# Kernel tuning notes

Measured on AMD Instinct MI355X. Metric: run time of the kernel, lower is better.

Reference implementation:

```python
import jax, jax.numpy as jnp
import numpy as np

B, C, T, W, H = 32, 80, 2048, 128, 512
FRAMES_PER_WORD = T // W  # 16
K = 5  # conv kernel size (Component approximated as Conv1d(k=5)+ReLU)


def conv1d(x, w, b):
    # x: [B, Cin, T], w: [Cout, Cin, K] -> [B, Cout, T] (SAME padding)
    y = jax.lax.conv_general_dilated(
        x, w, window_strides=(1,), padding='SAME',
        dimension_numbers=('NCH', 'OIH', 'NCH'))
    return y + b[None, :, None]


def setup_inputs() -> dict:
    key = jax.random.key(0)
    k1, k2, k3 = jax.random.split(key, 3)
    features = jax.random.normal(k1, (B, C, T), dtype=jnp.float32)
    # word bounds: contiguous equal-length spans [start, end) covering all T frames
    starts = (jnp.arange(W, dtype=jnp.int64) * FRAMES_PER_WORD)
    ends = starts + FRAMES_PER_WORD
    word_bounds = jnp.broadcast_to(jnp.stack([starts, ends])[None], (B, 2, W))
    word_lengths = jnp.full((B,), W, dtype=jnp.int64)
    enc_w = jax.random.normal(k2, (H, C, K), dtype=jnp.float32) * 0.02
    enc_b = jnp.zeros((H,), dtype=jnp.float32)
    dec_w = jax.random.normal(k3, (1, H, K), dtype=jnp.float32) * 0.02
    dec_b = jnp.zeros((1,), dtype=jnp.float32)
    return {'features': features, 'word_bounds': word_bounds,
            'word_lengths': word_lengths, 'enc_w': enc_w, 'enc_b': enc_b,
            'dec_w': dec_w, 'dec_b': dec_b}


def reference(features, word_bounds, word_lengths, enc_w, enc_b, dec_w, dec_b):
    # Frame encoder: Conv1d + ReLU -> [B, H, T]
    frame_embedding = jax.nn.relu(conv1d(features, enc_w, enc_b))
    t = jnp.arange(T)
    start = word_bounds[:, 0, :]  # [B, W]
    end = word_bounds[:, 1, :]    # [B, W]
    # Ragged per-word mean pooling, fused as a masked matmul (segment mean).
    mask = (t[None, None, :] >= start[..., None]) & (t[None, None, :] < end[..., None])  # [B, W, T]
    valid = jnp.arange(W)[None, :] < word_lengths[:, None]  # [B, W]
    maskf = (mask & valid[..., None]).astype(frame_embedding.dtype)
    counts = jnp.maximum(maskf.sum(-1), 1.0)  # [B, W]
    word_embeddings = jnp.einsum('bct,bwt->bcw', frame_embedding, maskf) / counts[:, None, :]
    # Word decoder: Conv1d over the word axis -> [B, 1, W]
    return conv1d(word_embeddings, dec_w, dec_b)
```

## Files before the change

### kernel.cpp

```cpp
#include <hip/hip_runtime.h>

#define B_ 32
#define C_ 80
#define T_ 2048
#define W_ 128
#define H_ 512
#define K_ 5

#define KTOT 400
#define KPAD 416
#define NKI  13
#define TM   128
#define TN   128
#define SF_STRIDE 88
#define SF_ROWS   136
#define ITER_STRIDE (2 * 4 * 64 * 8)
#define BF_ELEMS  (4 * NKI * ITER_STRIDE)

#define RB_FEAT   1024
#define RB_BFRAG  (RB_FEAT + BF_ELEMS / 256)
#define RB_WORDS  (RB_BFRAG + B_)
#define RB_WZERO  (RB_WORDS + 128)

typedef _Float16 half8 __attribute__((ext_vector_type(8)));
typedef float    f4v   __attribute__((ext_vector_type(4)));

__global__ __launch_bounds__(256) void prep_all(
    const float* __restrict__ feat, const float* __restrict__ enc_w,
    const int* __restrict__ bounds, const int* __restrict__ lengths,
    _Float16* __restrict__ featT, _Float16* __restrict__ Bf,
    int* __restrict__ word_of, float* __restrict__ inv_cnt,
    float* __restrict__ wemb)
{
    __shared__ _Float16 tile[64 * 80];
    const int bid = blockIdx.x;
    const int tid = threadIdx.x;

    if (bid < RB_FEAT) {
        const int b = bid >> 5, tc = bid & 31;
        const int t0 = tc * 64;
        for (int idx = tid; idx < 80 * 64; idx += 256) {
            int cc = idx >> 6, tt = idx & 63;
            float v = feat[((size_t)b * C_ + cc) * T_ + t0 + tt];
            tile[tt * 80 + cc] = (_Float16)v;
        }
        __syncthreads();
        for (int idx = tid; idx < 64 * 10; idx += 256) {
            int tt = idx / 10, g = idx % 10;
            *(f4v*)(featT + ((size_t)b * T_ + t0 + tt) * C_ + g * 8) =
                *(const f4v*)(tile + tt * 80 + g * 8);
        }
    } else if (bid < RB_BFRAG) {
        int idx = (bid - RB_FEAT) * 256 + tid;
        int e  = idx & 7;
        int l  = (idx >> 3) & 63;
        int j  = (idx >> 9) & 3;
        int w2 = (idx >> 11) & 1;
        int it = (idx >> 12) % NKI;
        int nt = idx / (NKI << 12);
        int h  = nt * 128 + w2 * 64 + j * 16 + (l & 15);
        int kc = it * 32 + (l >> 4) * 8 + e;
        float v = 0.f;
        if (kc < KTOT) v = enc_w[(h * C_ + kc % 80) * K_ + kc / 80];
        Bf[idx] = (_Float16)v;
    } else if (bid < RB_WORDS) {
        const int b = bid - RB_BFRAG;
        int* wob = word_of + b * T_;
        for (int t = tid; t < T_; t += 256) wob[t] = -1;
        __syncthreads();
        if (tid < W_) {
            const int len = lengths[b];
            int s = bounds[(b * 2 + 0) * W_ + tid];
            int e = bounds[(b * 2 + 1) * W_ + tid];
            s = max(s, 0); e = min(e, T_);
            bool valid = (tid < len) && (e > s);
            inv_cnt[b * W_ + tid] = valid ? 1.f / (float)(e - s) : 0.f;
            if (valid)
                for (int t = s; t < e; ++t) wob[t] = tid;
        }
    } else {
        f4v* wz = (f4v*)wemb;
        int base = (bid - RB_WORDS) * 256 + tid;
        for (int i = base; i < (B_ * W_ * H_) / 4; i += 128 * 256) wz[i] = (f4v){};
    }
}

__global__ __launch_bounds__(256, 3) void gemm_enc(
    const _Float16* __restrict__ featT,
    const _Float16* __restrict__ Bf,
    const float*    __restrict__ enc_b,
    const int*      __restrict__ word_of,
    const float*    __restrict__ inv_cnt,
    float*          __restrict__ wemb)
{
    __shared__ _Float16 sf[SF_ROWS * SF_STRIDE];

    const int tid = threadIdx.x;
    const int bid = blockIdx.x;
    const int nt = bid & 3;
    const int mt = (bid >> 2) & 15;
    const int b  = bid >> 6;
    const int t0 = mt * TM;
    const int h0 = nt * TN;

    const _Float16* fb = featT + (size_t)b * T_ * C_;
    for (int idx = tid; idx < SF_ROWS * 10; idx += 256) {
        int tt = idx / 10, g = idx % 10;
        int t = t0 - 2 + tt;
        int tcl = min(max(t, 0), T_ - 1);
        f4v v = {};
        if (t >= 0 && t < T_) v = *(const f4v*)(fb + tcl * C_ + g * 8);
        *(f4v*)(sf + tt * SF_STRIDE + g * 8) = v;
    }

    const int lane = tid & 63;
    const int wid  = tid >> 6;
    const int wm = (wid >> 1) * 64;
    const int wn = (wid & 1) * 64;
    const int w2 = wid & 1;
    const int ml = lane & 15;
    const int q  = lane >> 4;

    const half8* bfp = (const half8*)(Bf + (((nt * NKI) * 2 + w2) * 4 * 64 + lane) * 8);

    f4v acc[4][4] = {};

    __syncthreads();

    int c = q * 8;
    int aoff = (wm + ml) * SF_STRIDE + c;

    half8 bcur[4];
    #pragma unroll
    for (int j = 0; j < 4; ++j) bcur[j] = bfp[j * 64];

    for (int it = 0; it < NKI; ++it) {
        half8 bnext[4];
        {
            const half8* bn = bfp + (it + 1) * (2 * 4 * 64);
            #pragma unroll
            for (int j = 0; j < 4; ++j) bnext[j] = bn[j * 64];
        }
        half8 af[4];
        #pragma unroll
        for (int i = 0; i < 4; ++i)
            af[i] = *(const half8*)(sf + aoff + i * 16 * SF_STRIDE);
        #pragma unroll
        for (int i = 0; i < 4; ++i)
            #pragma unroll
            for (int j = 0; j < 4; ++j)
                acc[i][j] = __builtin_amdgcn_mfma_f32_16x16x32_f16(af[i], bcur[j], acc[i][j], 0, 0, 0);
        #pragma unroll
        for (int j = 0; j < 4; ++j) bcur[j] = bnext[j];
        aoff += 32; c += 32;
        if (c >= 80) { c -= 80; aoff += 8; }
    }

    const int bT = b * T_;
    const int bW = b * W_;
    float bias[4];
    #pragma unroll
    for (int j = 0; j < 4; ++j) bias[j] = enc_b[h0 + wn + j * 16 + ml];

    #pragma unroll
    for (int i = 0; i < 4; ++i) {
        const int tg = t0 + wm + i * 16;
        const int w0  = word_of[bT + tg];
        const int w15 = word_of[bT + tg + 15];
        if (w0 == w15) {
            if (w0 >= 0) {
                const float inv = inv_cnt[bW + w0];
                const bool own_lo = (tg == 0) || (word_of[bT + tg - 1] != w0);
                const bool own_hi = (tg + 16 >= T_) || (word_of[bT + tg + 16] != w0);
                #pragma unroll
                for (int j = 0; j < 4; ++j) {
                    float s = 0.f;
                    #pragma unroll
                    for (int r = 0; r < 4; ++r) s += fmaxf(acc[i][j][r] + bias[j], 0.f);
                    s += __shfl_down(s, 32, 64);
                    s += __shfl_down(s, 16, 64);
                    if (q == 0) {
                        float val = s * inv;
                        float* dst = &wemb[(size_t)(bW + w0) * H_ + h0 + wn + j * 16 + ml];
                        if (own_lo && own_hi) *dst = val;
                        else atomicAdd(dst, val);
                    }
                }
            }
        } else {
            #pragma unroll
            for (int j = 0; j < 4; ++j) {
                #pragma unroll
                for (int r = 0; r < 4; ++r) {
                    int t = tg + q * 4 + r;
                    int w = word_of[bT + t];
                    if (w >= 0)
                        atomicAdd(&wemb[(size_t)(bW + w) * H_ + h0 + wn + j * 16 + ml],
                                  fmaxf(acc[i][j][r] + bias[j], 0.f) * inv_cnt[bW + w]);
                }
            }
        }
    }
}

__global__ __launch_bounds__(256) void dec_all(const float* __restrict__ wemb,
                                               const float* __restrict__ dec_w,
                                               const float* __restrict__ dec_b,
                                               float* __restrict__ out) {
    __shared__ float sdw[H_ * K_];
    __shared__ float se[36][8];
    const int bid = blockIdx.x;
    const int b = bid >> 2, ch = bid & 3;
    const int w0 = ch * 32;
    for (int idx = threadIdx.x; idx < H_ * K_; idx += 256) sdw[idx] = dec_w[idx];
    __syncthreads();
    const int wid = threadIdx.x >> 6, lane = threadIdx.x & 63;
    for (int row = wid; row < 36; row += 4) {
        int wq = w0 - 2 + row;
        float a[K_] = {};
        if (wq >= 0 && wq < W_) {
            const float* src = wemb + ((size_t)b * W_ + wq) * H_;
            #pragma unroll
            for (int r = 0; r < H_ / 64; ++r) {
                int h = r * 64 + lane;
                float v = src[h];
                #pragma unroll
                for (int k = 0; k < K_; ++k) a[k] += v * sdw[h * K_ + k];
            }
        }
        #pragma unroll
        for (int k = 0; k < K_; ++k) {
            #pragma unroll
            for (int off = 32; off > 0; off >>= 1) a[k] += __shfl_down(a[k], off, 64);
        }
        if (lane == 0) {
            #pragma unroll
            for (int k = 0; k < K_; ++k) se[row][k] = a[k];
        }
    }
    __syncthreads();
    if (threadIdx.x < 32) {
        int wl = threadIdx.x;
        float acc = dec_b[0];
        #pragma unroll
        for (int k = 0; k < K_; ++k) acc += se[wl + k][k];
        out[b * W_ + w0 + wl] = acc;
    }
}

extern "C" void kernel_launch(void* const* d_in, const int* in_sizes, int n_in,
                              void* d_out, int out_size, void* d_ws, size_t ws_size,
                              hipStream_t stream) {
    const float* feat    = (const float*)d_in[0];
    const int*   bounds  = (const int*)  d_in[1];
    const int*   lengths = (const int*)  d_in[2];
    const float* enc_w   = (const float*)d_in[3];
    const float* enc_b   = (const float*)d_in[4];
    const float* dec_w   = (const float*)d_in[5];
    const float* dec_b   = (const float*)d_in[6];
    float* out = (float*)d_out;

    char* p = (char*)d_ws;
    _Float16* featT = (_Float16*)p;  p += (size_t)B_ * T_ * C_ * 2;
    _Float16* Bf    = (_Float16*)p;  p += (size_t)(BF_ELEMS + ITER_STRIDE) * 2;
    int* word_of    = (int*)p;       p += (size_t)B_ * T_ * 4;
    float* inv_cnt  = (float*)p;     p += (size_t)B_ * W_ * 4;
    float* wemb     = (float*)p;

    prep_all<<<RB_WZERO, 256, 0, stream>>>(feat, enc_w, bounds, lengths,
                                           featT, Bf, word_of, inv_cnt, wemb);
    gemm_enc<<<B_ * (T_ / TM) * (H_ / TN), 256, 0, stream>>>(
        featT, Bf, enc_b, word_of, inv_cnt, wemb);
    dec_all<<<B_ * 4, 256, 0, stream>>>(wemb, dec_w, dec_b, out);
}
```

Measured before the change: 130.0 us.

## Loop all N tiles per block and switch to 32x32x16 MFMA

The encoder GEMM now runs one block per (batch, 128-frame tile) and loops over all four 128-wide H tiles inside the block. The feature tile is staged in shared memory once and reused across every output column instead of being reloaded by four separate blocks. The MFMA shape moves from 16x16x32 to 32x32x16, and the weight fragment layout in prep is regenerated to match. The grid shrinks by 4x, which cuts redundant LDS staging but reduces parallelism and drops the B-fragment prefetch double buffering.

```diff
diff --git a/kernel.cpp b/kernel.cpp
--- a/kernel.cpp
+++ b/kernel.cpp
@@ -8,14 +8,12 @@
 #define K_ 5
 
 #define KTOT 400
-#define KPAD 416
 #define NKI  13
 #define TM   128
 #define TN   128
 #define SF_STRIDE 88
 #define SF_ROWS   136
-#define ITER_STRIDE (2 * 4 * 64 * 8)
-#define BF_ELEMS  (4 * NKI * ITER_STRIDE)
+#define BF_ELEMS  (4 * NKI * 2 * 2 * 2 * 64 * 8)
 
 #define RB_FEAT   1024
 #define RB_BFRAG  (RB_FEAT + BF_ELEMS / 256)
@@ -24,6 +22,7 @@
 
 typedef _Float16 half8 __attribute__((ext_vector_type(8)));
 typedef float    f4v   __attribute__((ext_vector_type(4)));
+typedef float    f16v  __attribute__((ext_vector_type(16)));
 
 __global__ __launch_bounds__(256) void prep_all(
     const float* __restrict__ feat, const float* __restrict__ enc_w,
@@ -54,14 +53,15 @@
         int idx = (bid - RB_FEAT) * 256 + tid;
         int e  = idx & 7;
         int l  = (idx >> 3) & 63;
-        int j  = (idx >> 9) & 3;
-        int w2 = (idx >> 11) & 1;
+        int j  = (idx >> 9) & 1;
+        int w2 = (idx >> 10) & 1;
+        int h  = (idx >> 11) & 1;
         int it = (idx >> 12) % NKI;
         int nt = idx / (NKI << 12);
-        int h  = nt * 128 + w2 * 64 + j * 16 + (l & 15);
-        int kc = it * 32 + (l >> 4) * 8 + e;
+        int n  = nt * 128 + w2 * 64 + j * 32 + (l & 31);
+        int kc = it * 32 + h * 16 + (l >> 5) * 8 + e;
         float v = 0.f;
-        if (kc < KTOT) v = enc_w[(h * C_ + kc % 80) * K_ + kc / 80];
+        if (kc < KTOT) v = enc_w[(n * C_ + kc % 80) * K_ + kc / 80];
         Bf[idx] = (_Float16)v;
     } else if (bid < RB_WORDS) {
         const int b = bid - RB_BFRAG;
@@ -97,11 +97,9 @@
 
     const int tid = threadIdx.x;
     const int bid = blockIdx.x;
-    const int nt = bid & 3;
-    const int mt = (bid >> 2) & 15;
-    const int b  = bid >> 6;
+    const int mt = bid & 15;
+    const int b  = bid >> 4;
     const int t0 = mt * TM;
-    const int h0 = nt * TN;
 
     const _Float16* fb = featT + (size_t)b * T_ * C_;
     for (int idx = tid; idx < SF_ROWS * 10; idx += 256) {
@@ -115,88 +113,105 @@
 
     const int lane = tid & 63;
     const int wid  = tid >> 6;
-    const int wm = (wid >> 1) * 64;
-    const int wn = (wid & 1) * 64;
-    const int w2 = wid & 1;
-    const int ml = lane & 15;
-    const int q  = lane >> 4;
-
-    const half8* bfp = (const half8*)(Bf + (((nt * NKI) * 2 + w2) * 4 * 64 + lane) * 8);
-
-    f4v acc[4][4] = {};
-
-    __syncthreads();
-
-    int c = q * 8;
-    int aoff = (wm + ml) * SF_STRIDE + c;
-
-    half8 bcur[4];
-    #pragma unroll
-    for (int j = 0; j < 4; ++j) bcur[j] = bfp[j * 64];
-
-    for (int it = 0; it < NKI; ++it) {
-        half8 bnext[4];
-        {
-            const half8* bn = bfp + (it + 1) * (2 * 4 * 64);
-            #pragma unroll
-            for (int j = 0; j < 4; ++j) bnext[j] = bn[j * 64];
-        }
-        half8 af[4];
-        #pragma unroll
-        for (int i = 0; i < 4; ++i)
-            af[i] = *(const half8*)(sf + aoff + i * 16 * SF_STRIDE);
-        #pragma unroll
-        for (int i = 0; i < 4; ++i)
-            #pragma unroll
-            for (int j = 0; j < 4; ++j)
-                acc[i][j] = __builtin_amdgcn_mfma_f32_16x16x32_f16(af[i], bcur[j], acc[i][j], 0, 0, 0);
-        #pragma unroll
-        for (int j = 0; j < 4; ++j) bcur[j] = bnext[j];
-        aoff += 32; c += 32;
-        if (c >= 80) { c -= 80; aoff += 8; }
-    }
+    const int wm  = (wid >> 1) * 64;
+    const int wn0 = (wid & 1) * 64;
+    const int w2  = wid & 1;
+    const int l31 = lane & 31;
+    const int ls  = lane >> 5;
+    const int q8  = ls * 8;
 
     const int bT = b * T_;
     const int bW = b * W_;
-    float bias[4];
+    int wlo[4], whi[4];
     #pragma unroll
-    for (int j = 0; j < 4; ++j) bias[j] = enc_b[h0 + wn + j * 16 + ml];
-
-    #pragma unroll
-    for (int i = 0; i < 4; ++i) {
-        const int tg = t0 + wm + i * 16;
-        const int w0  = word_of[bT + tg];
-        const int w15 = word_of[bT + tg + 15];
-        if (w0 == w15) {
-            if (w0 >= 0) {
-                const float inv = inv_cnt[bW + w0];
-                const bool own_lo = (tg == 0) || (word_of[bT + tg - 1] != w0);
-                const bool own_hi = (tg + 16 >= T_) || (word_of[bT + tg + 16] != w0);
+    for (int g = 0; g < 4; ++g) {
+        const int tg = t0 + wm + g * 16;
+        wlo[g] = word_of[bT + tg];
+        whi[g] = word_of[bT + tg + 15];
+    }
+
+    __syncthreads();
+
+    const int rowbase = (wm + l31) * SF_STRIDE;
+    const half8* bfw = (const half8*)Bf + w2 * 128 + lane;
+
+    for (int nt = 0; nt < 4; ++nt) {
+        const half8* bptr = bfw + nt * (NKI * 512);
+        const int h0 = nt * TN;
+
+        f16v acc[2][2] = {};
+        int c0 = q8,       off0 = q8;
+        int c1 = 16 + q8,  off1 = 16 + q8;
+
+        #pragma unroll
+        for (int it = 0; it < NKI; ++it) {
+            half8 a0[2], a1[2], b0[2], b1[2];
+            #pragma unroll
+            for (int i = 0; i < 2; ++i) {
+                a0[i] = *(const half8*)(sf + rowbase + i * 32 * SF_STRIDE + off0);
+                a1[i] = *(const half8*)(sf + rowbase + i * 32 * SF_STRIDE + off1);
+            }
+            #pragma unroll
+            for (int j = 0; j < 2; ++j) {
+                b0[j] = bptr[it * 512 + j * 64];
+                b1[j] = bptr[it * 512 + 256 + j * 64];
+            }
+            #pragma unroll
+            for (int i = 0; i < 2; ++i)
                 #pragma unroll
-                for (int j = 0; j < 4; ++j) {
-                    float s = 0.f;
+                for (int j = 0; j < 2; ++j) {
+                    acc[i][j] = __builtin_amdgcn_mfma_f32_32x32x16_f16(a0[i], b0[j], acc[i][j], 0, 0, 0);
+                    acc[i][j] = __builtin_amdgcn_mfma_f32_32x32x16_f16(a1[i], b1[j], acc[i][j], 0, 0, 0);
+                }
+            c0 += 32; off0 += 32; if (c0 >= 80) { c0 -= 80; off0 += 8; }
+            c1 += 32; off1 += 32; if (c1 >= 80) { c1 -= 80; off1 += 8; }
+        }
+
+        float bias[2];
+        #pragma unroll
+        for (int j = 0; j < 2; ++j) bias[j] = enc_b[h0 + wn0 + j * 32 + l31];
+
+        #pragma unroll
+        for (int i = 0; i < 2; ++i) {
+            #pragma unroll
+            for (int h16 = 0; h16 < 2; ++h16) {
+                const int g = i * 2 + h16;
+                const int tg = t0 + wm + i * 32 + h16 * 16;
+                const int w0 = wlo[g], w15 = whi[g];
+                if (w0 == w15) {
+                    if (w0 >= 0) {
+                        const float inv = inv_cnt[bW + w0];
+                        const bool own_lo = (tg == 0) || (word_of[bT + tg - 1] != w0);
+                        const bool own_hi = (tg + 16 >= T_) || (word_of[bT + tg + 16] != w0);
+                        #pragma unroll
+                        for (int j = 0; j < 2; ++j) {
+                            float s = 0.f;
+                            #pragma unroll
+                            for (int r = 0; r < 8; ++r)
+                                s += fmaxf(acc[i][j][h16 * 8 + r] + bias[j], 0.f);
+                            s += __shfl_down(s, 32, 64);
+                            if (lane < 32) {
+                                float val = s * inv;
+                                float* dst = &wemb[(size_t)(bW + w0) * H_ + h0 + wn0 + j * 32 + lane];
+                                if (own_lo && own_hi) *dst = val;
+                                else atomicAdd(dst, val);
+                            }
+                        }
+                    }
+                } else {
                     #pragma unroll
-                    for (int r = 0; r < 4; ++r) s += fmaxf(acc[i][j][r] + bias[j], 0.f);
-                    s += __shfl_down(s, 32, 64);
-                    s += __shfl_down(s, 16, 64);
-                    if (q == 0) {
-                        float val = s * inv;
-                        float* dst = &wemb[(size_t)(bW + w0) * H_ + h0 + wn + j * 16 + ml];
-                        if (own_lo && own_hi) *dst = val;
-                        else atomicAdd(dst, val);
+                    for (int j = 0; j < 2; ++j) {
+                        #pragma unroll
+                        for (int r = 0; r < 8; ++r) {
+                            const int reg = h16 * 8 + r;
+                            const int row = (reg & 3) + 8 * (reg >> 2) + 4 * ls;
+                            const int t = t0 + wm + i * 32 + row;
+                            const int w = word_of[bT + t];
+                            if (w >= 0)
+                                atomicAdd(&wemb[(size_t)(bW + w) * H_ + h0 + wn0 + j * 32 + l31],
+                                          fmaxf(acc[i][j][reg] + bias[j], 0.f) * inv_cnt[bW + w]);
+                        }
                     }
-                }
-            }
-        } else {
-            #pragma unroll
-            for (int j = 0; j < 4; ++j) {
-                #pragma unroll
-                for (int r = 0; r < 4; ++r) {
-                    int t = tg + q * 4 + r;
-                    int w = word_of[bT + t];
-                    if (w >= 0)
-                        atomicAdd(&wemb[(size_t)(bW + w) * H_ + h0 + wn + j * 16 + ml],
-                                  fmaxf(acc[i][j][r] + bias[j], 0.f) * inv_cnt[bW + w]);
                 }
             }
         }
@@ -262,14 +277,14 @@
 
     char* p = (char*)d_ws;
     _Float16* featT = (_Float16*)p;  p += (size_t)B_ * T_ * C_ * 2;
-    _Float16* Bf    = (_Float16*)p;  p += (size_t)(BF_ELEMS + ITER_STRIDE) * 2;
+    _Float16* Bf    = (_Float16*)p;  p += (size_t)BF_ELEMS * 2;
     int* word_of    = (int*)p;       p += (size_t)B_ * T_ * 4;
     float* inv_cnt  = (float*)p;     p += (size_t)B_ * W_ * 4;
     float* wemb     = (float*)p;
 
     prep_all<<<RB_WZERO, 256, 0, stream>>>(feat, enc_w, bounds, lengths,
                                            featT, Bf, word_of, inv_cnt, wemb);
-    gemm_enc<<<B_ * (T_ / TM) * (H_ / TN), 256, 0, stream>>>(
+    gemm_enc<<<B_ * (T_ / TM), 256, 0, stream>>>(
         featT, Bf, enc_b, word_of, inv_cnt, wemb);
     dec_all<<<B_ * 4, 256, 0, stream>>>(wemb, dec_w, dec_b, out);
 }
```

Measured after the change: 207.7 us. 59.8% more time.
